# Kernel tuning notes

Hardware: AMD Instinct MI355X
Metric: run time of the kernel (lower is better)

Reference implementation:

```python
import jax, jax.numpy as jnp
import numpy as np
from jax import lax

# Quantized ConvBnA block: int8 conv with int32 accumulation, per-channel
# bias add (folded BN), power-of-two requant via arithmetic right shift,
# clamp, and narrow-int cast (uint8 since Act_min >= 0 -> pure_positive).

N, CIN, COUT, H, W, K = 32, 128, 256, 56, 56, 3

def setup_inputs() -> dict:
    key = jax.random.key(0)
    k1, k2, k3 = jax.random.split(key, 3)
    # int8-valued inputs / weights (stored as int32 per harness dtype support)
    x = jax.random.randint(k1, (N, CIN, H, W), -64, 64, dtype=jnp.int32)
    weight = jax.random.randint(k2, (COUT, CIN, K, K), -128, 128, dtype=jnp.int32)
    # BN_shift is negative (shift right by -n = 8 bits)
    n = jnp.full((1, COUT, 1, 1), -8, dtype=jnp.int32)
    # folded-BN integer bias, broadcasts over [N, C, H, W]
    t = jax.random.randint(k3, (1, COUT, 1, 1), -2048, 2048, dtype=jnp.int32)
    act_min = 0
    act_max = 255
    return {"x": x, "weight": weight, "n": n, "t": t,
            "act_min": act_min, "act_max": act_max}

def reference(x, weight, n, t, act_min, act_max):
    # int32-accumulated convolution (stride 1, pad 1, dilation 1, groups 1)
    acc = lax.conv_general_dilated(
        x.astype(jnp.int32), weight.astype(jnp.int32),
        window_strides=(1, 1), padding=((1, 1), (1, 1)),
        dimension_numbers=("NCHW", "OIHW", "NCHW"))
    acc = acc + t                              # folded-BN bias add
    acc = jnp.right_shift(acc, -n)             # pow2 requant, arithmetic shift
    acc = jnp.clip(acc, jnp.int32(act_min), jnp.int32(act_max))
    # pure_positive (Act_min >= 0) -> small unsigned type
    return acc.astype(jnp.uint8)
```

## Files before the change

kernel.cpp:

```cpp
#include <hip/hip_runtime.h>
#include <cstdint>


typedef __attribute__((ext_vector_type(8))) short short8;
typedef __attribute__((ext_vector_type(4))) float f32x4;

#define C_IN   128
#define C_OUT  256
#define HW2    3136
#define NPIX   100352
#define OUT_NSTRIDE 802816

#define XBF_BYTES 25690112
#define WBF_OFF   25690112
#define WBF_BYTES 589824
#define ZP_OFF    (WBF_OFF + WBF_BYTES)

__device__ __forceinline__ ushort f2bf(float f) {
  return (ushort)(__builtin_bit_cast(unsigned int, f) >> 16);
}

__device__ __forceinline__ void gload_lds16(const void* g, void* l) {
  __builtin_amdgcn_global_load_lds(
      (const __attribute__((address_space(1))) void*)(uintptr_t)g,
      (__attribute__((address_space(3))) void*)(uint32_t)(uintptr_t)l,
      16, 0, 0);
}

__global__ void wxform(const int* __restrict__ w, ushort* __restrict__ wbf,
                       float* __restrict__ zp) {
  int id = blockIdx.x * 256 + threadIdx.x;
  int ci  = id & 127;
  int co  = (id >> 7) & 255;
  int kwh = id >> 15;
  int v = w[co * 1152 + ci * 9 + kwh];
  wbf[id] = f2bf((float)v);
  if (blockIdx.x == 0 && threadIdx.x < 64) zp[threadIdx.x] = 0.0f;
}

__global__ __launch_bounds__(256) void xform(const int* __restrict__ x,
                                             ushort* __restrict__ xbf) {
  __shared__ ushort t[64][65];
  int bid = blockIdx.x;
  int hb = bid % 49;
  int tmp = bid / 49;
  int cb = tmp & 1;
  int n  = tmp >> 1;
  int tid = threadIdx.x;
  int c  = tid & 63;
  int r0 = tid >> 6;
  const int* src = x + n * (C_IN * HW2) + (cb * 64) * HW2 + hb * 64;
#pragma unroll
  for (int i = 0; i < 16; i++) {
    int r = r0 + i * 4;
    t[r][c] = f2bf((float)src[r * HW2 + c]);
  }
  __syncthreads();
  ushort* dst = xbf + n * (HW2 * C_IN) + (hb * 64) * C_IN + cb * 64;
#pragma unroll
  for (int i = 0; i < 16; i++) {
    int hwi = r0 + i * 4;
    dst[hwi * C_IN + c] = t[c][hwi];
  }
}

__global__ __launch_bounds__(256, 2) void conv_mfma(
    const ushort* __restrict__ xbf, const ushort* __restrict__ wbf,
    const ushort* __restrict__ zp,
    const int* __restrict__ nshift, const int* __restrict__ tbias,
    const int* __restrict__ aminp, const int* __restrict__ amaxp,
    int* __restrict__ out) {
  __shared__ char lds[65536];

  const int tid = threadIdx.x;
  const int bid = blockIdx.x;
  const int bm = bid & 1;
  const int pb = bid >> 1;
  const int l  = tid & 63;
  const int wid = tid >> 6;
  const int wm = wid >> 1, wn = wid & 1;

  const int chl = tid & 7;
  const int rsw = (tid >> 3) & 7;
  const int chg = chl ^ rsw;
  const int koff_sw = chg * 8;

  int p_idx[4], p_h[4], p_w[4];
#pragma unroll
  for (int i = 0; i < 4; i++) {
    int pr = (tid >> 3) + i * 32;
    int p  = pb * 128 + pr;
    int n  = p / HW2;
    int hw = p - n * HW2;
    int h  = hw / 56;
    int w  = hw - h * 56;
    p_idx[i] = p; p_h[i] = h; p_w[i] = w;
  }

  auto stageAB = [&](int g, int kt, int buf) {
    char* Ab = lds + buf * 32768;
    char* Bb = Ab + 16384;
    const int dh = g / 3 - 1, dw = g % 3 - 1;
    const int doff = dh * 56 + dw;
    const int kbase = kt * 64 + koff_sw;
    const ushort* wsrc = wbf + (g * 256 + bm * 128) * 128 + kbase;
#pragma unroll
    for (int i = 0; i < 4; i++) {
      int row = (tid >> 3) + i * 32;
      gload_lds16(wsrc + row * 128, Ab + (tid + i * 256) * 16);
    }
#pragma unroll
    for (int i = 0; i < 4; i++) {
      int h2 = p_h[i] + dh, w2 = p_w[i] + dw;
      bool valid = ((unsigned)h2 < 56u) && ((unsigned)w2 < 56u);
      const ushort* gp = valid ? (xbf + (p_idx[i] + doff) * 128 + kbase)
                               : (const ushort*)zp;
      gload_lds16(gp, Bb + (tid + i * 256) * 16);
    }
  };

  f32x4 acc[4][4] = {};
  const int lrow = l & 15;
  const int lk16 = (l >> 4) * 16;
  const int lsw  = (l & 7) << 4;

  auto computeStep = [&](int buf) {
    char* Ab = lds + buf * 32768;
    char* Bb = Ab + 16384;
#pragma unroll
    for (int kk = 0; kk < 2; kk++) {
      short8 a[4], b[4];
      const int cb = ((kk * 64 + lk16) ^ lsw);
#pragma unroll
      for (int mi = 0; mi < 4; mi++) {
        int row = wm * 64 + mi * 16 + lrow;
        a[mi] = *(const short8*)(Ab + row * 128 + cb);
      }
#pragma unroll
      for (int ni = 0; ni < 4; ni++) {
        int row = wn * 64 + ni * 16 + lrow;
        b[ni] = *(const short8*)(Bb + row * 128 + cb);
      }
#pragma unroll
      for (int mi = 0; mi < 4; mi++)
#pragma unroll
        for (int ni = 0; ni < 4; ni++)
          acc[mi][ni] = __builtin_amdgcn_mfma_f32_16x16x32_bf16(
              a[mi], b[ni], acc[mi][ni], 0, 0, 0);
    }
  };

  stageAB(0, 0, 0);
#pragma unroll 1
  for (int s = 0; s < 18; ++s) {
    const int s1 = s + 1;
    if (s1 < 18) stageAB(s1 >> 1, s1 & 1, s1 & 1);
    __builtin_amdgcn_sched_barrier(0);
    if (s1 < 18) { asm volatile("s_waitcnt vmcnt(8)" ::: "memory"); }
    else         { asm volatile("s_waitcnt vmcnt(0)" ::: "memory"); }
    __builtin_amdgcn_s_barrier();
    __builtin_amdgcn_sched_barrier(0);
    computeStep(s & 1);
    __builtin_amdgcn_sched_barrier(0);
    __builtin_amdgcn_s_barrier();
    __builtin_amdgcn_sched_barrier(0);
  }

  const int amin = aminp[0], amax = amaxp[0];
  int pbase[4];
#pragma unroll
  for (int ni = 0; ni < 4; ni++) {
    int p = pb * 128 + wn * 64 + ni * 16 + lrow;
    int n = p / HW2;
    int hw = p - n * HW2;
    pbase[ni] = n * OUT_NSTRIDE + hw;
  }
#pragma unroll
  for (int mi = 0; mi < 4; mi++) {
    int co0 = bm * 128 + wm * 64 + mi * 16 + ((l >> 4) << 2);
    const int4 t4 = *(const int4*)(tbias + co0);
    const int4 n4 = *(const int4*)(nshift + co0);
#pragma unroll
    for (int ni = 0; ni < 4; ni++) {
      f32x4 fr = acc[mi][ni];
#pragma unroll
      for (int r = 0; r < 4; r++) {
        int tv = (r == 0) ? t4.x : (r == 1) ? t4.y : (r == 2) ? t4.z : t4.w;
        int nv = (r == 0) ? n4.x : (r == 1) ? n4.y : (r == 2) ? n4.z : n4.w;
        int v = (int)fr[r] + tv;
        v = v >> (-nv);
        v = v < amin ? amin : (v > amax ? amax : v);
        out[pbase[ni] + (co0 + r) * HW2] = v;
      }
    }
  }
}

extern "C" void kernel_launch(void* const* d_in, const int* in_sizes, int n_in,
                              void* d_out, int out_size, void* d_ws, size_t ws_size,
                              hipStream_t stream) {
  const int* x      = (const int*)d_in[0];
  const int* w      = (const int*)d_in[1];
  const int* nshift = (const int*)d_in[2];
  const int* tbias  = (const int*)d_in[3];
  const int* aminp  = (const int*)d_in[4];
  const int* amaxp  = (const int*)d_in[5];
  int* out = (int*)d_out;

  ushort* xbf = (ushort*)d_ws;
  ushort* wbf = (ushort*)((char*)d_ws + WBF_OFF);
  ushort* zp  = (ushort*)((char*)d_ws + ZP_OFF);

  hipLaunchKernelGGL(wxform, dim3(1152), dim3(256), 0, stream, w, wbf, (float*)zp);
  hipLaunchKernelGGL(xform,  dim3(3136), dim3(256), 0, stream, x, xbf);
  hipLaunchKernelGGL(conv_mfma, dim3(1568), dim3(256), 0, stream,
                     xbf, wbf, zp, nshift, tbias, aminp, amaxp, out);
}
```

Before: 214.0 us.

## Switch conv to int8 MFMA with packed int8 staging of inputs and weights

Replaces bf16 conversion and the bf16 MFMA with int8 packing and the i32 16x16x64 i8 MFMA. This halves staged bytes and the number of K-steps (9 instead of 18). The input transform also drops the LDS transpose in favour of direct register packing. Accumulation becomes exact int32, which removes any float rounding concern. The risk is a new uncoalesced store pattern in xform and the LDS swizzle having to match the new 64-wide i8 K layout.

```diff
diff --git a/kernel.cpp b/kernel.cpp
--- a/kernel.cpp
+++ b/kernel.cpp
@@ -2,23 +2,18 @@
 #include <cstdint>
 
 
-typedef __attribute__((ext_vector_type(8))) short short8;
-typedef __attribute__((ext_vector_type(4))) float f32x4;
+typedef __attribute__((ext_vector_type(4))) int i32x4;
+typedef __attribute__((ext_vector_type(2))) int i32x2;
 
 #define C_IN   128
 #define C_OUT  256
 #define HW2    3136
-#define NPIX   100352
 #define OUT_NSTRIDE 802816
 
-#define XBF_BYTES 25690112
-#define WBF_OFF   25690112
-#define WBF_BYTES 589824
-#define ZP_OFF    (WBF_OFF + WBF_BYTES)
-
-__device__ __forceinline__ ushort f2bf(float f) {
-  return (ushort)(__builtin_bit_cast(unsigned int, f) >> 16);
-}
+#define XQ_BYTES 12845056
+#define WQ_OFF   XQ_BYTES
+#define WQ_BYTES 294912
+#define ZP_OFF   (WQ_OFF + WQ_BYTES)
 
 __device__ __forceinline__ void gload_lds16(const void* g, void* l) {
   __builtin_amdgcn_global_load_lds(
@@ -27,46 +22,44 @@
       16, 0, 0);
 }
 
-__global__ void wxform(const int* __restrict__ w, ushort* __restrict__ wbf,
-                       float* __restrict__ zp) {
+__global__ void wxform(const int* __restrict__ w, char* __restrict__ wq,
+                       int* __restrict__ zp) {
   int id = blockIdx.x * 256 + threadIdx.x;
-  int ci  = id & 127;
-  int co  = (id >> 7) & 255;
-  int kwh = id >> 15;
-  int v = w[co * 1152 + ci * 9 + kwh];
-  wbf[id] = f2bf((float)v);
-  if (blockIdx.x == 0 && threadIdx.x < 64) zp[threadIdx.x] = 0.0f;
+  int ci = id & 127;
+  int co = (id >> 7) & 255;
+  int g  = id >> 15;
+  wq[id] = (char)w[co * 1152 + ci * 9 + g];
+  if (blockIdx.x == 0 && threadIdx.x < 64) zp[threadIdx.x] = 0;
 }
 
 __global__ __launch_bounds__(256) void xform(const int* __restrict__ x,
-                                             ushort* __restrict__ xbf) {
-  __shared__ ushort t[64][65];
+                                             char* __restrict__ xq) {
   int bid = blockIdx.x;
   int hb = bid % 49;
-  int tmp = bid / 49;
-  int cb = tmp & 1;
-  int n  = tmp >> 1;
-  int tid = threadIdx.x;
-  int c  = tid & 63;
-  int r0 = tid >> 6;
-  const int* src = x + n * (C_IN * HW2) + (cb * 64) * HW2 + hb * 64;
-#pragma unroll
-  for (int i = 0; i < 16; i++) {
-    int r = r0 + i * 4;
-    t[r][c] = f2bf((float)src[r * HW2 + c]);
-  }
-  __syncthreads();
-  ushort* dst = xbf + n * (HW2 * C_IN) + (hb * 64) * C_IN + cb * 64;
-#pragma unroll
-  for (int i = 0; i < 16; i++) {
-    int hwi = r0 + i * 4;
-    dst[hwi * C_IN + c] = t[c][hwi];
+  int n  = bid / 49;
+  int t  = threadIdx.x;
+  int cig = t & 15;
+  int hw0 = (t >> 4) * 4;
+  const int* src = x + n * (C_IN * HW2) + hb * 64 + hw0;
+  i32x4 ld[8];
+#pragma unroll
+  for (int j = 0; j < 8; j++)
+    ld[j] = *(const i32x4*)(src + (cig * 8 + j) * HW2);
+  char* dst = xq + (size_t)(n * HW2 + hb * 64 + hw0) * 128 + cig * 8;
+#pragma unroll
+  for (int p = 0; p < 4; p++) {
+    unsigned lo = (ld[0][p] & 255) | ((ld[1][p] & 255) << 8) |
+                  ((ld[2][p] & 255) << 16) | ((unsigned)(ld[3][p] & 255) << 24);
+    unsigned hi = (ld[4][p] & 255) | ((ld[5][p] & 255) << 8) |
+                  ((ld[6][p] & 255) << 16) | ((unsigned)(ld[7][p] & 255) << 24);
+    i32x2 v; v[0] = (int)lo; v[1] = (int)hi;
+    *(i32x2*)(dst + p * 128) = v;
   }
 }
 
 __global__ __launch_bounds__(256, 2) void conv_mfma(
-    const ushort* __restrict__ xbf, const ushort* __restrict__ wbf,
-    const ushort* __restrict__ zp,
+    const char* __restrict__ xq, const char* __restrict__ wq,
+    const char* __restrict__ zp,
     const int* __restrict__ nshift, const int* __restrict__ tbias,
     const int* __restrict__ aminp, const int* __restrict__ amaxp,
     int* __restrict__ out) {
@@ -83,7 +76,7 @@
   const int chl = tid & 7;
   const int rsw = (tid >> 3) & 7;
   const int chg = chl ^ rsw;
-  const int koff_sw = chg * 8;
+  const int kboff = chg * 16;
 
   int p_idx[4], p_h[4], p_w[4];
 #pragma unroll
@@ -97,31 +90,30 @@
     p_idx[i] = p; p_h[i] = h; p_w[i] = w;
   }
 
-  auto stageAB = [&](int g, int kt, int buf) {
+  auto stageAB = [&](int g, int buf) {
     char* Ab = lds + buf * 32768;
     char* Bb = Ab + 16384;
     const int dh = g / 3 - 1, dw = g % 3 - 1;
     const int doff = dh * 56 + dw;
-    const int kbase = kt * 64 + koff_sw;
-    const ushort* wsrc = wbf + (g * 256 + bm * 128) * 128 + kbase;
+    const char* wsrc = wq + (((g * 256 + bm * 128)) << 7) + kboff;
 #pragma unroll
     for (int i = 0; i < 4; i++) {
       int row = (tid >> 3) + i * 32;
-      gload_lds16(wsrc + row * 128, Ab + (tid + i * 256) * 16);
+      gload_lds16(wsrc + (row << 7), Ab + (tid + i * 256) * 16);
     }
 #pragma unroll
     for (int i = 0; i < 4; i++) {
       int h2 = p_h[i] + dh, w2 = p_w[i] + dw;
       bool valid = ((unsigned)h2 < 56u) && ((unsigned)w2 < 56u);
-      const ushort* gp = valid ? (xbf + (p_idx[i] + doff) * 128 + kbase)
-                               : (const ushort*)zp;
+      const char* gp = valid ? (xq + ((size_t)(p_idx[i] + doff) << 7) + kboff)
+                             : zp;
       gload_lds16(gp, Bb + (tid + i * 256) * 16);
     }
   };
 
-  f32x4 acc[4][4] = {};
+  i32x4 acc[4][4] = {};
   const int lrow = l & 15;
-  const int lk16 = (l >> 4) * 16;
+  const int lk   = (l >> 4) * 16;
   const int lsw  = (l & 7) << 4;
 
   auto computeStep = [&](int buf) {
@@ -129,35 +121,35 @@
     char* Bb = Ab + 16384;
 #pragma unroll
     for (int kk = 0; kk < 2; kk++) {
-      short8 a[4], b[4];
-      const int cb = ((kk * 64 + lk16) ^ lsw);
+      i32x4 a[4], b[4];
+      const int cb = ((kk * 64 + lk) ^ lsw);
 #pragma unroll
       for (int mi = 0; mi < 4; mi++) {
         int row = wm * 64 + mi * 16 + lrow;
-        a[mi] = *(const short8*)(Ab + row * 128 + cb);
+        a[mi] = *(const i32x4*)(Ab + (row << 7) + cb);
       }
 #pragma unroll
       for (int ni = 0; ni < 4; ni++) {
         int row = wn * 64 + ni * 16 + lrow;
-        b[ni] = *(const short8*)(Bb + row * 128 + cb);
+        b[ni] = *(const i32x4*)(Bb + (row << 7) + cb);
       }
 #pragma unroll
       for (int mi = 0; mi < 4; mi++)
 #pragma unroll
         for (int ni = 0; ni < 4; ni++)
-          acc[mi][ni] = __builtin_amdgcn_mfma_f32_16x16x32_bf16(
+          acc[mi][ni] = __builtin_amdgcn_mfma_i32_16x16x64_i8(
               a[mi], b[ni], acc[mi][ni], 0, 0, 0);
     }
   };
 
-  stageAB(0, 0, 0);
+  stageAB(0, 0);
 #pragma unroll 1
-  for (int s = 0; s < 18; ++s) {
+  for (int s = 0; s < 9; ++s) {
     const int s1 = s + 1;
-    if (s1 < 18) stageAB(s1 >> 1, s1 & 1, s1 & 1);
-    __builtin_amdgcn_sched_barrier(0);
-    if (s1 < 18) { asm volatile("s_waitcnt vmcnt(8)" ::: "memory"); }
-    else         { asm volatile("s_waitcnt vmcnt(0)" ::: "memory"); }
+    if (s1 < 9) stageAB(s1, s1 & 1);
+    __builtin_amdgcn_sched_barrier(0);
+    if (s1 < 9) { asm volatile("s_waitcnt vmcnt(8)" ::: "memory"); }
+    else        { asm volatile("s_waitcnt vmcnt(0)" ::: "memory"); }
     __builtin_amdgcn_s_barrier();
     __builtin_amdgcn_sched_barrier(0);
     computeStep(s & 1);
@@ -182,12 +174,11 @@
     const int4 n4 = *(const int4*)(nshift + co0);
 #pragma unroll
     for (int ni = 0; ni < 4; ni++) {
-      f32x4 fr = acc[mi][ni];
 #pragma unroll
       for (int r = 0; r < 4; r++) {
         int tv = (r == 0) ? t4.x : (r == 1) ? t4.y : (r == 2) ? t4.z : t4.w;
         int nv = (r == 0) ? n4.x : (r == 1) ? n4.y : (r == 2) ? n4.z : n4.w;
-        int v = (int)fr[r] + tv;
+        int v = acc[mi][ni][r] + tv;
         v = v >> (-nv);
         v = v < amin ? amin : (v > amax ? amax : v);
         out[pbase[ni] + (co0 + r) * HW2] = v;
@@ -207,12 +198,12 @@
   const int* amaxp  = (const int*)d_in[5];
   int* out = (int*)d_out;
 
-  ushort* xbf = (ushort*)d_ws;
-  ushort* wbf = (ushort*)((char*)d_ws + WBF_OFF);
-  ushort* zp  = (ushort*)((char*)d_ws + ZP_OFF);
-
-  hipLaunchKernelGGL(wxform, dim3(1152), dim3(256), 0, stream, w, wbf, (float*)zp);
-  hipLaunchKernelGGL(xform,  dim3(3136), dim3(256), 0, stream, x, xbf);
+  char* xq = (char*)d_ws;
+  char* wq = (char*)d_ws + WQ_OFF;
+  char* zp = (char*)d_ws + ZP_OFF;
+
+  hipLaunchKernelGGL(wxform, dim3(1152), dim3(256), 0, stream, w, wq, (int*)zp);
+  hipLaunchKernelGGL(xform,  dim3(1568), dim3(256), 0, stream, x, xq);
   hipLaunchKernelGGL(conv_mfma, dim3(1568), dim3(256), 0, stream,
-                     xbf, wbf, zp, nshift, tbias, aminp, amaxp, out);
-}
+                     xq, wq, zp, nshift, tbias, aminp, amaxp, out);
+}
```

After: 186.0 us. 13.1% less time.
